# Kernel optimization log

Hardware: AMD Instinct MI355X
Metric: run time of the kernel (lower is better)

The kernel has to match this reference:

```python
import jax, jax.numpy as jnp
import numpy as np

NUM_HEADS = 16
HIDDEN = 1024
HEAD = HIDDEN // NUM_HEADS
NEG_INF = -10000.0


def setup_inputs() -> dict:
    key = jax.random.key(0)
    k1, k2, k3, k4 = jax.random.split(key, 4)
    B, S = 4, 2048
    x = jax.random.normal(k1, (B, S, HIDDEN), dtype=jnp.float32)
    pos_embeds = jax.random.normal(k2, (S, HIDDEN), dtype=jnp.float32)
    # Dense(3*hidden, use_bias=False) and Dense(hidden, use_bias=False)
    Wqkv = jax.random.normal(k3, (HIDDEN, 3 * HIDDEN), dtype=jnp.float32) / np.sqrt(HIDDEN)
    Wo = jax.random.normal(k4, (HIDDEN, HIDDEN), dtype=jnp.float32) / np.sqrt(HIDDEN)
    return {"x": x, "pos_embeds": pos_embeds, "Wqkv": Wqkv, "Wo": Wo}


def _compute_qkv(t, Wqkv):
    # rearrange '... s (k n h) -> k ... n s h', k=3, n=NUM_HEADS
    proj = t @ Wqkv  # [..., s, 3*n*h]
    proj = proj.reshape(*t.shape[:-1], 3, NUM_HEADS, HEAD)  # [..., s, 3, n, h]
    # move: k first, then leading dims, then n, s, h
    nd = proj.ndim
    perm = (nd - 3,) + tuple(range(nd - 4)) + (nd - 2, nd - 4, nd - 1)
    return jnp.transpose(proj, perm)  # [3, ..., n, s, h]


def reference(x, pos_embeds, Wqkv, Wo):
    S = x.shape[-2]
    q, k, v = _compute_qkv(x, Wqkv)  # each [B, n, S, h]
    pos_qkv = _compute_qkv(pos_embeds[:S], Wqkv)  # [3, n, S, h]
    pos_q, pos_k = pos_qkv[0], pos_qkv[1]
    q = q + pos_q  # broadcast over batch
    k = k + pos_k
    scores = jnp.einsum('bnqh,bnkh->bnqk', q, k) / np.sqrt(HEAD).astype(np.float32)
    causal = jnp.arange(S)[:, None] < jnp.arange(S)[None, :]  # strict upper triangle (future)
    scores = jnp.where(causal, NEG_INF, scores)
    probs = jax.nn.softmax(scores, axis=-1)
    # dropout deterministic (training=False) -> identity
    combined = jnp.einsum('bnqk,bnkh->bnqh', probs, v)  # [B, n, S, h]
    combined = jnp.transpose(combined, (0, 2, 1, 3)).reshape(x.shape[0], S, HIDDEN)  # '... n q h -> ... q (n h)'
    out = combined @ Wo
    return out
```

## Files before the change

### kernel.cpp

```cpp
#include <hip/hip_runtime.h>


typedef float f32x4 __attribute__((ext_vector_type(4)));
typedef short bf16x8 __attribute__((ext_vector_type(8)));
typedef short bf16x4 __attribute__((ext_vector_type(4)));

#define MFMA_BF16(a, b, c) __builtin_amdgcn_mfma_f32_16x16x32_bf16((a), (b), (c), 0, 0, 0)

#if __has_builtin(__builtin_amdgcn_mfma_f32_16x16x16bf16_1k)
#define HAVE_MFMA16 1
#define MFMA_BF16_K16(a, b, c) __builtin_amdgcn_mfma_f32_16x16x16bf16_1k((a), (b), (c), 0, 0, 0)
#else
#define HAVE_MFMA16 0
#endif

__device__ __forceinline__ short f2bf(float f) {
  union { float f; unsigned u; } v; v.f = f;
  unsigned u = v.u;
  u += 0x7fffu + ((u >> 16) & 1u);
  return (short)(u >> 16);
}

__device__ __forceinline__ float bf2f(short s) {
  union { unsigned u; float f; } v;
  v.u = ((unsigned)(unsigned short)s) << 16;
  return v.f;
}

__device__ __forceinline__ int cvt_pk_bf16(float lo, float hi) {
  int r;
  asm("v_cvt_pk_bf16_f32 %0, %1, %2" : "=v"(r) : "v"(lo), "v"(hi));
  return r;
}

__device__ __forceinline__ int swzK(int row, int colbyte) {
  return row * 64 + (((colbyte) ^ ((row & 7) << 4)) >> 1);
}
__device__ __forceinline__ int swzV(int row, int colbyte) {
  return row * 64 + ((((colbyte >> 3) + row) & 15) << 2);
}

__device__ const int QT_X[30] = {5,6,7,8,9,10,11,11,12,12,13,13,14,14,15,15,
                                 4,10, 3,9,15, 2,8,14, 1,7,13, 0,6,12};
__device__ const int CH_X[30] = {0,0,0,0,0,0,0,1,0,1,0,1,0,1,0,1,
                                 0,1, 0,1,2, 0,1,2, 0,1,2, 0,1,2};
__device__ const int START_QT[16] = {0,1,2,3,4,5,6,8,10,12,14,16,18,21,24,27};

__global__ __launch_bounds__(256) void prep_x(const float* __restrict__ x,
                                              const float* __restrict__ pos,
                                              short* __restrict__ xb,
                                              short* __restrict__ xpb) {
  int i = blockIdx.x * 256 + threadIdx.x;
  int idx = i * 4;
  const float4 xv = *(const float4*)(x + idx);
  const float4 pv = *(const float4*)(pos + (idx & ((2048 * 1024) - 1)));
  short4 a, b;
  a.x = f2bf(xv.x); a.y = f2bf(xv.y); a.z = f2bf(xv.z); a.w = f2bf(xv.w);
  b.x = f2bf(xv.x + pv.x); b.y = f2bf(xv.y + pv.y);
  b.z = f2bf(xv.z + pv.z); b.w = f2bf(xv.w + pv.w);
  *(short4*)(xb + idx) = a;
  *(short4*)(xpb + idx) = b;
}

__global__ __launch_bounds__(256) void transpose_w(const float* __restrict__ in,
                                                   short* __restrict__ out,
                                                   int K, int N) {
  __shared__ float tile[32][33];
  int n0 = blockIdx.x * 32, k0 = blockIdx.y * 32;
  int c = threadIdx.x & 31, r0 = threadIdx.x >> 5;
  for (int i = 0; i < 4; i++) {
    int r = r0 + i * 8;
    tile[r][c] = in[(size_t)(k0 + r) * N + n0 + c];
  }
  __syncthreads();
  for (int i = 0; i < 4; i++) {
    int r = r0 + i * 8;
    out[(size_t)(n0 + r) * K + k0 + c] = f2bf(tile[c][r]);
  }
}

__global__ __launch_bounds__(256) void gemm_qkv(const short* __restrict__ xb,
                                                const short* __restrict__ xpb,
                                                const short* __restrict__ wt,
                                                short* __restrict__ qg,
                                                short* __restrict__ kg,
                                                short* __restrict__ vtg) {
  __shared__ __align__(16) short As[128 * 72];
  __shared__ __align__(16) short Bs[128 * 72];
  const int n = blockIdx.x;
  const int idx = n >> 3;
  const int bm = (n & 7) * 8 + (idx & 7);
  const int bn = idx >> 3;
  const short* __restrict__ A = (bn < 16) ? xpb : xb;
  const int tid = threadIdx.x;
  const int lane = tid & 63, wid = tid >> 6;
  const int wm = wid & 1, wn = wid >> 1;
  const int quad = lane >> 4, l16 = lane & 15;
  const f32x4 fzero = {0.f, 0.f, 0.f, 0.f};
  f32x4 acc[4][4];
  for (int mt = 0; mt < 4; mt++)
    for (int nt = 0; nt < 4; nt++) acc[mt][nt] = fzero;
  const int arow0 = bm * 128, brow0 = bn * 128;
  for (int k0 = 0; k0 < 1024; k0 += 64) {
    for (int i = 0; i < 4; i++) {
      int cc = tid + i * 256;
      int r = cc >> 3, kc = cc & 7;
      *(int4*)(As + r * 72 + kc * 8) =
          *(const int4*)(A + (size_t)(arow0 + r) * 1024 + k0 + kc * 8);
      *(int4*)(Bs + r * 72 + kc * 8) =
          *(const int4*)(wt + (size_t)(brow0 + r) * 1024 + k0 + kc * 8);
    }
    __syncthreads();
    for (int ks = 0; ks < 2; ks++) {
      bf16x8 af[4], bfr[4];
      for (int mt = 0; mt < 4; mt++)
        af[mt] = *(const bf16x8*)(As + (wm * 64 + mt * 16 + l16) * 72 + ks * 32 + quad * 8);
      for (int nt = 0; nt < 4; nt++)
        bfr[nt] = *(const bf16x8*)(Bs + (wn * 64 + nt * 16 + l16) * 72 + ks * 32 + quad * 8);
      for (int mt = 0; mt < 4; mt++)
        for (int nt = 0; nt < 4; nt++)
          acc[mt][nt] = MFMA_BF16(af[mt], bfr[nt], acc[mt][nt]);
    }
    __syncthreads();
  }
  for (int nt = 0; nt < 4; nt++) {
    int col = bn * 128 + wn * 64 + nt * 16 + l16;
    int kk = col >> 10, head = (col >> 6) & 15, hh = col & 63;
    for (int mt = 0; mt < 4; mt++) {
      int rowb = bm * 128 + wm * 64 + mt * 16 + quad * 4;
      int b = rowb >> 11, s0 = rowb & 2047;
      if (kk == 2) {
        short4 sv;
        sv.x = f2bf(acc[mt][nt][0]); sv.y = f2bf(acc[mt][nt][1]);
        sv.z = f2bf(acc[mt][nt][2]); sv.w = f2bf(acc[mt][nt][3]);
        *(short4*)(vtg + (size_t)((b * 16 + head) * 64 + hh) * 2048 + s0) = sv;
      } else {
        short* __restrict__ dst = (kk == 0) ? qg : kg;
        float scale = (kk == 0) ? 0.18033688f : 1.0f;
        for (int r = 0; r < 4; r++)
          dst[(size_t)((b * 16 + head) * 2048 + s0 + r) * 64 + hh] =
              f2bf(acc[mt][nt][r] * scale);
      }
    }
  }
}

__global__ __launch_bounds__(256, 3) void attn_part(const short* __restrict__ qg,
                                                    const short* __restrict__ kg,
                                                    const short* __restrict__ vtg,
                                                    short* __restrict__ pO,
                                                    float* __restrict__ pL) {
  const int n = blockIdx.x;
  const int i = n >> 3;
  const int bh = (n & 7) * 8 + i / 30;
  const int slot = i % 30;
  const int qt = QT_X[slot], ch = CH_X[slot];
  const int p = bh * 30 + START_QT[qt] + ch;
  const short* __restrict__ Q = qg + (size_t)bh * 2048 * 64;
  const short* __restrict__ K = kg + (size_t)bh * 2048 * 64;
  const short* __restrict__ VT = vtg + (size_t)bh * 64 * 2048;
  __shared__ __align__(16) short Ks[2][64 * 64];
  __shared__ __align__(16) short Vs[2][64 * 64];
#if !HAVE_MFMA16
  __shared__ __align__(16) short Ps[4][16 * 72];
#endif
  const int tid = threadIdx.x, lane = tid & 63, w = tid >> 6;
  const int quad = lane >> 4, l16 = lane & 15;
  const f32x4 fzero = {0.f, 0.f, 0.f, 0.f};

  bf16x8 bq[2][2];
#pragma unroll
  for (int sub = 0; sub < 2; sub++) {
    int qrow = qt * 128 + w * 32 + sub * 16 + l16;
#pragma unroll
    for (int ks = 0; ks < 2; ks++)
      bq[sub][ks] = *(const bf16x8*)(Q + (size_t)qrow * 64 + ks * 32 + quad * 8);
  }
  f32x4 acco[2][4];
  f32x4 lrun[2];
#pragma unroll
  for (int sub = 0; sub < 2; sub++) {
    for (int nt = 0; nt < 4; nt++) acco[sub][nt] = fzero;
    lrun[sub] = fzero;
  }

  const int kt0 = ch * 12;
  const int kt1 = min(kt0 + 12, 2 * qt + 2);
  const int qmin_w = qt * 128 + w * 32;

  const int sr0 = tid >> 3, sr1 = sr0 + 32;
  const int scs = (tid & 7) * 8;
  const int scb = (tid & 7) * 16;
  const int oK0 = swzK(sr0, scb), oK1 = swzK(sr1, scb);
  const int oV0a = swzV(sr0, scb), oV0b = swzV(sr0, scb + 8);
  const int oV1a = swzV(sr1, scb), oV1b = swzV(sr1, scb + 8);

  int4 kreg[2], vreg[2];
  {
    int kv0 = kt0 * 64;
    kreg[0] = *(const int4*)(K + (size_t)(kv0 + sr0) * 64 + scs);
    kreg[1] = *(const int4*)(K + (size_t)(kv0 + sr1) * 64 + scs);
    vreg[0] = *(const int4*)(VT + (size_t)sr0 * 2048 + kv0 + scs);
    vreg[1] = *(const int4*)(VT + (size_t)sr1 * 2048 + kv0 + scs);
    *(int4*)(&Ks[0][oK0]) = kreg[0];
    *(int4*)(&Ks[0][oK1]) = kreg[1];
    *(int2*)(&Vs[0][oV0a]) = make_int2(vreg[0].x, vreg[0].y);
    *(int2*)(&Vs[0][oV0b]) = make_int2(vreg[0].z, vreg[0].w);
    *(int2*)(&Vs[0][oV1a]) = make_int2(vreg[1].x, vreg[1].y);
    *(int2*)(&Vs[0][oV1b]) = make_int2(vreg[1].z, vreg[1].w);
  }
  __syncthreads();

  for (int kt = kt0; kt < kt1; kt++) {
    const int cur = (kt - kt0) & 1;
    if (kt + 1 < kt1) {
      int kv0 = (kt + 1) * 64;
      kreg[0] = *(const int4*)(K + (size_t)(kv0 + sr0) * 64 + scs);
      kreg[1] = *(const int4*)(K + (size_t)(kv0 + sr1) * 64 + scs);
      vreg[0] = *(const int4*)(VT + (size_t)sr0 * 2048 + kv0 + scs);
      vreg[1] = *(const int4*)(VT + (size_t)sr1 * 2048 + kv0 + scs);
    }

    if (kt * 64 <= qmin_w + 31) {
      f32x4 accs[2][4];
#pragma unroll
      for (int sub = 0; sub < 2; sub++)
        for (int nt = 0; nt < 4; nt++) accs[sub][nt] = fzero;
      __builtin_amdgcn_s_setprio(1);
#pragma unroll
      for (int ks = 0; ks < 2; ks++)
#pragma unroll
        for (int nt = 0; nt < 4; nt++) {
          bf16x8 ak = *(const bf16x8*)(&Ks[cur][swzK(nt * 16 + l16, ks * 64 + quad * 16)]);
          accs[0][nt] = MFMA_BF16(ak, bq[0][ks], accs[0][nt]);
          accs[1][nt] = MFMA_BF16(ak, bq[1][ks], accs[1][nt]);
        }
      __builtin_amdgcn_s_setprio(0);

      if ((kt + 1) * 64 > qmin_w) {
#pragma unroll
        for (int sub = 0; sub < 2; sub++) {
          int q = qmin_w + sub * 16 + l16;
#pragma unroll
          for (int nt = 0; nt < 4; nt++) {
            int kv = kt * 64 + nt * 16 + quad * 4;
#pragma unroll
            for (int r = 0; r < 4; r++)
              if (kv + r > q) accs[sub][nt][r] = -1e30f;
          }
        }
      }

#pragma unroll
      for (int sub = 0; sub < 2; sub++)
#pragma unroll
        for (int nt = 0; nt < 4; nt++) {
#pragma unroll
          for (int r = 0; r < 4; r++) accs[sub][nt][r] = exp2f(accs[sub][nt][r]);
          lrun[sub] += accs[sub][nt];
        }

#if HAVE_MFMA16
      __builtin_amdgcn_s_setprio(1);
#pragma unroll
      for (int kk = 0; kk < 4; kk++) {
        union { int2 i2; bf16x4 v; } p0, p1;
        p0.i2.x = cvt_pk_bf16(accs[0][kk][0], accs[0][kk][1]);
        p0.i2.y = cvt_pk_bf16(accs[0][kk][2], accs[0][kk][3]);
        p1.i2.x = cvt_pk_bf16(accs[1][kk][0], accs[1][kk][1]);
        p1.i2.y = cvt_pk_bf16(accs[1][kk][2], accs[1][kk][3]);
#pragma unroll
        for (int nth = 0; nth < 4; nth++) {
          bf16x4 av = *(const bf16x4*)(&Vs[cur][swzV(nth * 16 + l16, kk * 32 + quad * 8)]);
          acco[0][nth] = MFMA_BF16_K16(av, p0.v, acco[0][nth]);
          acco[1][nth] = MFMA_BF16_K16(av, p1.v, acco[1][nth]);
        }
      }
      __builtin_amdgcn_s_setprio(0);
#else
      short* P = Ps[w];
#pragma unroll
      for (int sub = 0; sub < 2; sub++) {
#pragma unroll
        for (int nt = 0; nt < 4; nt++) {
          int2 pk;
          pk.x = cvt_pk_bf16(accs[sub][nt][0], accs[sub][nt][1]);
          pk.y = cvt_pk_bf16(accs[sub][nt][2], accs[sub][nt][3]);
          *(int2*)(P + l16 * 72 + nt * 16 + quad * 4) = pk;
        }
#pragma unroll
        for (int ks2 = 0; ks2 < 2; ks2++) {
          bf16x8 bp = *(const bf16x8*)(P + l16 * 72 + ks2 * 32 + quad * 8);
#pragma unroll
          for (int nth = 0; nth < 4; nth++) {
            int r = nth * 16 + l16;
            int4 t4;
            *(int2*)&t4.x = *(const int2*)(&Vs[cur][swzV(r, ks2 * 64 + quad * 16)]);
            *(int2*)&t4.z = *(const int2*)(&Vs[cur][swzV(r, ks2 * 64 + quad * 16 + 8)]);
            bf16x8 av = *(const bf16x8*)&t4;
            acco[sub][nth] = MFMA_BF16(av, bp, acco[sub][nth]);
          }
        }
      }
#endif
    }

    if (kt + 1 < kt1) {
      const int nxt = cur ^ 1;
      *(int4*)(&Ks[nxt][oK0]) = kreg[0];
      *(int4*)(&Ks[nxt][oK1]) = kreg[1];
      *(int2*)(&Vs[nxt][oV0a]) = make_int2(vreg[0].x, vreg[0].y);
      *(int2*)(&Vs[nxt][oV0b]) = make_int2(vreg[0].z, vreg[0].w);
      *(int2*)(&Vs[nxt][oV1a]) = make_int2(vreg[1].x, vreg[1].y);
      *(int2*)(&Vs[nxt][oV1b]) = make_int2(vreg[1].z, vreg[1].w);
    }
    __syncthreads();
  }

#pragma unroll
  for (int sub = 0; sub < 2; sub++) {
    float lh = (lrun[sub][0] + lrun[sub][1]) + (lrun[sub][2] + lrun[sub][3]);
    lh += __shfl_xor(lh, 16);
    lh += __shfl_xor(lh, 32);
    int qloc = w * 32 + sub * 16 + l16;
    if (quad == 0) pL[p * 128 + qloc] = lh;
  }

  short* Ob = &Ks[0][0];
#pragma unroll
  for (int sub = 0; sub < 2; sub++) {
    int qloc = w * 32 + sub * 16 + l16;
#pragma unroll
    for (int nth = 0; nth < 4; nth++) {
      int2 pk;
      pk.x = cvt_pk_bf16(acco[sub][nth][0], acco[sub][nth][1]);
      pk.y = cvt_pk_bf16(acco[sub][nth][2], acco[sub][nth][3]);
      *(int2*)(Ob + swzK(qloc, nth * 32 + quad * 8)) = pk;
    }
  }
  __syncthreads();
  {
    const int row = tid >> 1;
    const int hb = (tid & 1) * 64;
    int4 v0 = *(const int4*)(Ob + swzK(row, hb));
    int4 v1 = *(const int4*)(Ob + swzK(row, hb + 16));
    int4 v2 = *(const int4*)(Ob + swzK(row, hb + 32));
    int4 v3 = *(const int4*)(Ob + swzK(row, hb + 48));
    int4* dst = (int4*)(pO + (size_t)p * 8192 + tid * 32);
    dst[0] = v0; dst[1] = v1; dst[2] = v2; dst[3] = v3;
  }
}

__global__ __launch_bounds__(256) void attn_merge(const short* __restrict__ pO,
                                                  const float* __restrict__ pL,
                                                  short* __restrict__ comb) {
  const int n = blockIdx.x;
  const int i = n >> 3;
  const int bh = (n & 7) * 8 + (i >> 4);
  const int qt = i & 15;
  const int head = bh & 15, b = bh >> 4;
  const int nch = (2 * qt + 13) / 12;
  const int p0 = bh * 30 + START_QT[qt];
  const int t = threadIdx.x;
  const int qloc = t >> 1, hh = (t & 1) * 32;

  float l = 0.f;
  for (int c = 0; c < nch; c++) l += pL[(p0 + c) * 128 + qloc];
  const float inv = 1.f / l;

  float acc[32];
#pragma unroll
  for (int j = 0; j < 32; j++) acc[j] = 0.f;
  for (int c = 0; c < nch; c++) {
    const short* src = pO + (size_t)(p0 + c) * 8192 + (size_t)qloc * 64 + hh;
#pragma unroll
    for (int v = 0; v < 4; v++) {
      short4 d0 = *(const short4*)(src + v * 8);
      short4 d1 = *(const short4*)(src + v * 8 + 4);
      acc[v * 8 + 0] += bf2f(d0.x); acc[v * 8 + 1] += bf2f(d0.y);
      acc[v * 8 + 2] += bf2f(d0.z); acc[v * 8 + 3] += bf2f(d0.w);
      acc[v * 8 + 4] += bf2f(d1.x); acc[v * 8 + 5] += bf2f(d1.y);
      acc[v * 8 + 6] += bf2f(d1.z); acc[v * 8 + 7] += bf2f(d1.w);
    }
  }
  size_t base = (size_t)(b * 2048 + qt * 128 + qloc) * 1024 + head * 64 + hh;
#pragma unroll
  for (int v = 0; v < 8; v++) {
    short4 sv;
    sv.x = f2bf(acc[v * 4 + 0] * inv);
    sv.y = f2bf(acc[v * 4 + 1] * inv);
    sv.z = f2bf(acc[v * 4 + 2] * inv);
    sv.w = f2bf(acc[v * 4 + 3] * inv);
    *(short4*)(comb + base + v * 4) = sv;
  }
}

__global__ __launch_bounds__(256) void gemm_out(const short* __restrict__ A,
                                                const short* __restrict__ wt,
                                                float* __restrict__ out) {
  __shared__ __align__(16) short As[128 * 72];
  __shared__ __align__(16) short Bs[128 * 72];
  const int n = blockIdx.x;
  const int idx = n >> 3;
  const int bm = (n & 7) * 8 + (idx & 7);
  const int bn = idx >> 3;
  const int tid = threadIdx.x;
  const int lane = tid & 63, wid = tid >> 6;
  const int wm = wid & 1, wn = wid >> 1;
  const int quad = lane >> 4, l16 = lane & 15;
  const f32x4 fzero = {0.f, 0.f, 0.f, 0.f};
  f32x4 acc[4][4];
  for (int mt = 0; mt < 4; mt++)
    for (int nt = 0; nt < 4; nt++) acc[mt][nt] = fzero;
  const int arow0 = bm * 128, brow0 = bn * 128;
  for (int k0 = 0; k0 < 1024; k0 += 64) {
    for (int i = 0; i < 4; i++) {
      int cc = tid + i * 256;
      int r = cc >> 3, kc = cc & 7;
      *(int4*)(As + r * 72 + kc * 8) =
          *(const int4*)(A + (size_t)(arow0 + r) * 1024 + k0 + kc * 8);
      *(int4*)(Bs + r * 72 + kc * 8) =
          *(const int4*)(wt + (size_t)(brow0 + r) * 1024 + k0 + kc * 8);
    }
    __syncthreads();
    for (int ks = 0; ks < 2; ks++) {
      bf16x8 af[4], bfr[4];
      for (int mt = 0; mt < 4; mt++)
        af[mt] = *(const bf16x8*)(As + (wm * 64 + mt * 16 + l16) * 72 + ks * 32 + quad * 8);
      for (int nt = 0; nt < 4; nt++)
        bfr[nt] = *(const bf16x8*)(Bs + (wn * 64 + nt * 16 + l16) * 72 + ks * 32 + quad * 8);
      for (int mt = 0; mt < 4; mt++)
        for (int nt = 0; nt < 4; nt++)
          acc[mt][nt] = MFMA_BF16(af[mt], bfr[nt], acc[mt][nt]);
    }
    __syncthreads();
  }
  for (int nt = 0; nt < 4; nt++) {
    int col = bn * 128 + wn * 64 + nt * 16 + l16;
    for (int mt = 0; mt < 4; mt++) {
      int rowb = bm * 128 + wm * 64 + mt * 16 + quad * 4;
      for (int r = 0; r < 4; r++)
        out[(size_t)(rowb + r) * 1024 + col] = acc[mt][nt][r];
    }
  }
}

extern "C" void kernel_launch(void* const* d_in, const int* in_sizes, int n_in,
                              void* d_out, int out_size, void* d_ws, size_t ws_size,
                              hipStream_t stream) {
  const float* x    = (const float*)d_in[0];
  const float* pos  = (const float*)d_in[1];
  const float* Wqkv = (const float*)d_in[2];
  const float* Wo   = (const float*)d_in[3];
  float* out = (float*)d_out;

  char* ws = (char*)d_ws;
  const size_t SZ = (size_t)8192 * 1024 * 2;
  short* xb    = (short*)(ws);
  short* xpb   = (short*)(ws + SZ);
  short* pO    = (short*)(ws);
  float* pL    = (float*)(ws + (size_t)1920 * 8192 * 2);
  short* q     = (short*)(ws + 2 * SZ);
  short* k     = (short*)(ws + 3 * SZ);
  short* vt    = (short*)(ws + 4 * SZ);
  short* comb  = (short*)(ws + 5 * SZ);
  short* wqkvt = (short*)(ws + 6 * SZ);
  short* wot   = (short*)(ws + 6 * SZ + (size_t)3072 * 1024 * 2);

  prep_x<<<8192, 256, 0, stream>>>(x, pos, xb, xpb);
  transpose_w<<<dim3(96, 32), 256, 0, stream>>>(Wqkv, wqkvt, 1024, 3072);
  transpose_w<<<dim3(32, 32), 256, 0, stream>>>(Wo, wot, 1024, 1024);
  gemm_qkv<<<dim3(1536), 256, 0, stream>>>(xb, xpb, wqkvt, q, k, vt);
  attn_part<<<dim3(1920), 256, 0, stream>>>(q, k, vt, pO, pL);
  attn_merge<<<dim3(1024), 256, 0, stream>>>(pO, pL, comb);
  gemm_out<<<dim3(512), 256, 0, stream>>>(comb, wot, out);
}
```

Before: 293.7 us.

## Stage QKV GEMM epilogue through LDS and single-buffer attention K/V tiles

The QKV GEMM epilogue now writes accumulators into shared memory and then emits coalesced 16-byte rows to Q, K and transposed V, replacing scattered 2-byte and 8-byte global stores. The attention kernel drops its double-buffered K/V shared tiles for a single buffer, with an extra barrier each iteration, which halves its LDS footprint and may allow more resident blocks. exp2f is replaced with the hardware exp2 builtin. The trade-off is an added sync per KV tile and less overlap between LDS stores and compute.

```diff
diff --git a/kernel.cpp b/kernel.cpp
--- a/kernel.cpp
+++ b/kernel.cpp
@@ -25,6 +25,14 @@
   union { unsigned u; float f; } v;
   v.u = ((unsigned)(unsigned short)s) << 16;
   return v.f;
+}
+
+__device__ __forceinline__ float fast_exp2(float x) {
+#if __has_builtin(__builtin_amdgcn_exp2f)
+  return __builtin_amdgcn_exp2f(x);
+#else
+  return exp2f(x);
+#endif
 }
 
 __device__ __forceinline__ int cvt_pk_bf16(float lo, float hi) {
@@ -85,8 +93,9 @@
                                                 short* __restrict__ qg,
                                                 short* __restrict__ kg,
                                                 short* __restrict__ vtg) {
-  __shared__ __align__(16) short As[128 * 72];
-  __shared__ __align__(16) short Bs[128 * 72];
+  __shared__ __align__(16) short Sh[2][128 * 72];
+  short* As = &Sh[0][0];
+  short* Bs = &Sh[1][0];
   const int n = blockIdx.x;
   const int idx = n >> 3;
   const int bm = (n & 7) * 8 + (idx & 7);
@@ -123,25 +132,52 @@
     }
     __syncthreads();
   }
-  for (int nt = 0; nt < 4; nt++) {
-    int col = bn * 128 + wn * 64 + nt * 16 + l16;
-    int kk = col >> 10, head = (col >> 6) & 15, hh = col & 63;
-    for (int mt = 0; mt < 4; mt++) {
-      int rowb = bm * 128 + wm * 64 + mt * 16 + quad * 4;
-      int b = rowb >> 11, s0 = rowb & 2047;
-      if (kk == 2) {
-        short4 sv;
-        sv.x = f2bf(acc[mt][nt][0]); sv.y = f2bf(acc[mt][nt][1]);
-        sv.z = f2bf(acc[mt][nt][2]); sv.w = f2bf(acc[mt][nt][3]);
-        *(short4*)(vtg + (size_t)((b * 16 + head) * 64 + hh) * 2048 + s0) = sv;
-      } else {
-        short* __restrict__ dst = (kk == 0) ? qg : kg;
-        float scale = (kk == 0) ? 0.18033688f : 1.0f;
-        for (int r = 0; r < 4; r++)
-          dst[(size_t)((b * 16 + head) * 2048 + s0 + r) * 64 + hh] =
-              f2bf(acc[mt][nt][r] * scale);
+
+  short* Sf = &Sh[0][0];
+  const int kk = bn >> 3;
+  const int bglob = (bm * 128) >> 11;
+  const int s0v = (bm * 128) & 2047;
+  if (kk == 2) {
+#pragma unroll
+    for (int mt = 0; mt < 4; mt++)
+#pragma unroll
+      for (int nt = 0; nt < 4; nt++) {
+        int col = wn * 64 + nt * 16 + l16;
+        int sb = wm * 64 + mt * 16 + quad * 4;
+        int2 pk;
+        pk.x = cvt_pk_bf16(acc[mt][nt][0], acc[mt][nt][1]);
+        pk.y = cvt_pk_bf16(acc[mt][nt][2], acc[mt][nt][3]);
+        *(int2*)(Sf + col * 136 + sb) = pk;
       }
-    }
+    __syncthreads();
+    const int col = tid >> 1, half = tid & 1;
+    const short* src = Sf + col * 136 + half * 64;
+    int head = (bn * 2 + (col >> 6)) & 15;
+    int hh = col & 63;
+    int4* dst = (int4*)(vtg + (size_t)((bglob * 16 + head) * 64 + hh) * 2048 + s0v + half * 64);
+#pragma unroll
+    for (int c = 0; c < 8; c++) dst[c] = *(const int4*)(src + c * 8);
+  } else {
+    const float scale = (kk == 0) ? 0.18033688f : 1.0f;
+#pragma unroll
+    for (int mt = 0; mt < 4; mt++)
+#pragma unroll
+      for (int nt = 0; nt < 4; nt++) {
+        int col = wn * 64 + nt * 16 + l16;
+#pragma unroll
+        for (int r = 0; r < 4; r++) {
+          int s_loc = wm * 64 + mt * 16 + quad * 4 + r;
+          Sf[s_loc * 136 + col] = f2bf(acc[mt][nt][r] * scale);
+        }
+      }
+    __syncthreads();
+    const int row = tid >> 1, half = tid & 1;
+    const short* src = Sf + row * 136 + half * 64;
+    int head = (bn * 2 + half) & 15;
+    short* __restrict__ dstp = (kk == 0) ? qg : kg;
+    int4* dst = (int4*)(dstp + (size_t)((bglob * 16 + head) * 2048 + s0v + row) * 64);
+#pragma unroll
+    for (int c = 0; c < 8; c++) dst[c] = *(const int4*)(src + c * 8);
   }
 }
 
@@ -159,8 +195,9 @@
   const short* __restrict__ Q = qg + (size_t)bh * 2048 * 64;
   const short* __restrict__ K = kg + (size_t)bh * 2048 * 64;
   const short* __restrict__ VT = vtg + (size_t)bh * 64 * 2048;
-  __shared__ __align__(16) short Ks[2][64 * 64];
-  __shared__ __align__(16) short Vs[2][64 * 64];
+  __shared__ __align__(16) short KV[2][64 * 64];
+  short* Ks = &KV[0][0];
+  short* Vs = &KV[1][0];
 #if !HAVE_MFMA16
   __shared__ __align__(16) short Ps[4][16 * 72];
 #endif
@@ -202,17 +239,18 @@
     kreg[1] = *(const int4*)(K + (size_t)(kv0 + sr1) * 64 + scs);
     vreg[0] = *(const int4*)(VT + (size_t)sr0 * 2048 + kv0 + scs);
     vreg[1] = *(const int4*)(VT + (size_t)sr1 * 2048 + kv0 + scs);
-    *(int4*)(&Ks[0][oK0]) = kreg[0];
-    *(int4*)(&Ks[0][oK1]) = kreg[1];
-    *(int2*)(&Vs[0][oV0a]) = make_int2(vreg[0].x, vreg[0].y);
-    *(int2*)(&Vs[0][oV0b]) = make_int2(vreg[0].z, vreg[0].w);
-    *(int2*)(&Vs[0][oV1a]) = make_int2(vreg[1].x, vreg[1].y);
-    *(int2*)(&Vs[0][oV1b]) = make_int2(vreg[1].z, vreg[1].w);
-  }
-  __syncthreads();
+  }
 
   for (int kt = kt0; kt < kt1; kt++) {
-    const int cur = (kt - kt0) & 1;
+    if (kt > kt0) __syncthreads();
+    *(int4*)(&Ks[oK0]) = kreg[0];
+    *(int4*)(&Ks[oK1]) = kreg[1];
+    *(int2*)(&Vs[oV0a]) = make_int2(vreg[0].x, vreg[0].y);
+    *(int2*)(&Vs[oV0b]) = make_int2(vreg[0].z, vreg[0].w);
+    *(int2*)(&Vs[oV1a]) = make_int2(vreg[1].x, vreg[1].y);
+    *(int2*)(&Vs[oV1b]) = make_int2(vreg[1].z, vreg[1].w);
+    __syncthreads();
+
     if (kt + 1 < kt1) {
       int kv0 = (kt + 1) * 64;
       kreg[0] = *(const int4*)(K + (size_t)(kv0 + sr0) * 64 + scs);
@@ -231,7 +269,7 @@
       for (int ks = 0; ks < 2; ks++)
 #pragma unroll
         for (int nt = 0; nt < 4; nt++) {
-          bf16x8 ak = *(const bf16x8*)(&Ks[cur][swzK(nt * 16 + l16, ks * 64 + quad * 16)]);
+          bf16x8 ak = *(const bf16x8*)(&Ks[swzK(nt * 16 + l16, ks * 64 + quad * 16)]);
           accs[0][nt] = MFMA_BF16(ak, bq[0][ks], accs[0][nt]);
           accs[1][nt] = MFMA_BF16(ak, bq[1][ks], accs[1][nt]);
         }
@@ -256,22 +294,22 @@
 #pragma unroll
         for (int nt = 0; nt < 4; nt++) {
 #pragma unroll
-          for (int r = 0; r < 4; r++) accs[sub][nt][r] = exp2f(accs[sub][nt][r]);
+          for (int r = 0; r < 4; r++) accs[sub][nt][r] = fast_exp2(accs[sub][nt][r]);
           lrun[sub] += accs[sub][nt];
         }
 
 #if HAVE_MFMA16
       __builtin_amdgcn_s_setprio(1);
 #pragma unroll
-      for (int kk = 0; kk < 4; kk++) {
+      for (int kkk = 0; kkk < 4; kkk++) {
         union { int2 i2; bf16x4 v; } p0, p1;
-        p0.i2.x = cvt_pk_bf16(accs[0][kk][0], accs[0][kk][1]);
-        p0.i2.y = cvt_pk_bf16(accs[0][kk][2], accs[0][kk][3]);
-        p1.i2.x = cvt_pk_bf16(accs[1][kk][0], accs[1][kk][1]);
-        p1.i2.y = cvt_pk_bf16(accs[1][kk][2], accs[1][kk][3]);
+        p0.i2.x = cvt_pk_bf16(accs[0][kkk][0], accs[0][kkk][1]);
+        p0.i2.y = cvt_pk_bf16(accs[0][kkk][2], accs[0][kkk][3]);
+        p1.i2.x = cvt_pk_bf16(accs[1][kkk][0], accs[1][kkk][1]);
+        p1.i2.y = cvt_pk_bf16(accs[1][kkk][2], accs[1][kkk][3]);
 #pragma unroll
         for (int nth = 0; nth < 4; nth++) {
-          bf16x4 av = *(const bf16x4*)(&Vs[cur][swzV(nth * 16 + l16, kk * 32 + quad * 8)]);
+          bf16x4 av = *(const bf16x4*)(&Vs[swzV(nth * 16 + l16, kkk * 32 + quad * 8)]);
           acco[0][nth] = MFMA_BF16_K16(av, p0.v, acco[0][nth]);
           acco[1][nth] = MFMA_BF16_K16(av, p1.v, acco[1][nth]);
         }
@@ -295,8 +333,8 @@
           for (int nth = 0; nth < 4; nth++) {
             int r = nth * 16 + l16;
             int4 t4;
-            *(int2*)&t4.x = *(const int2*)(&Vs[cur][swzV(r, ks2 * 64 + quad * 16)]);
-            *(int2*)&t4.z = *(const int2*)(&Vs[cur][swzV(r, ks2 * 64 + quad * 16 + 8)]);
+            *(int2*)&t4.x = *(const int2*)(&Vs[swzV(r, ks2 * 64 + quad * 16)]);
+            *(int2*)&t4.z = *(const int2*)(&Vs[swzV(r, ks2 * 64 + quad * 16 + 8)]);
             bf16x8 av = *(const bf16x8*)&t4;
             acco[sub][nth] = MFMA_BF16(av, bp, acco[sub][nth]);
           }
@@ -304,17 +342,6 @@
       }
 #endif
     }
-
-    if (kt + 1 < kt1) {
-      const int nxt = cur ^ 1;
-      *(int4*)(&Ks[nxt][oK0]) = kreg[0];
-      *(int4*)(&Ks[nxt][oK1]) = kreg[1];
-      *(int2*)(&Vs[nxt][oV0a]) = make_int2(vreg[0].x, vreg[0].y);
-      *(int2*)(&Vs[nxt][oV0b]) = make_int2(vreg[0].z, vreg[0].w);
-      *(int2*)(&Vs[nxt][oV1a]) = make_int2(vreg[1].x, vreg[1].y);
-      *(int2*)(&Vs[nxt][oV1b]) = make_int2(vreg[1].z, vreg[1].w);
-    }
-    __syncthreads();
   }
 
 #pragma unroll
@@ -326,7 +353,8 @@
     if (quad == 0) pL[p * 128 + qloc] = lh;
   }
 
-  short* Ob = &Ks[0][0];
+  __syncthreads();
+  short* Ob = &KV[0][0];
 #pragma unroll
   for (int sub = 0; sub < 2; sub++) {
     int qloc = w * 32 + sub * 16 + l16;
```

Result: no change. 292.1 us (-0.6%).
